# Kernel optimization log

Hardware: AMD Instinct MI355X
Metric: run time of the kernel (lower is better)

## Reference

```python
import jax, jax.numpy as jnp
import numpy as np

E = 1024   # embed_dim
H = 16     # num_heads
D = E // H # head_dim
T = 1024   # tgt_len
S = 1024   # src_len
B = 2      # batch
DELTA = 1.0
SCALE = D ** -0.5


def setup_inputs() -> dict:
    key = jax.random.key(0)
    ks = jax.random.split(key, 16)
    def lin(k, o, i):
        return jax.random.normal(k, (o, i), dtype=jnp.float32) / np.float32(np.sqrt(i))
    return {
        'query': jax.random.normal(ks[0], (T, B, E), dtype=jnp.float32),
        'key_in': jax.random.normal(ks[1], (S, B, E), dtype=jnp.float32),
        'value': jax.random.normal(ks[2], (S, B, E), dtype=jnp.float32),
        'Wq': lin(ks[3], E, E), 'bq': jnp.zeros((E,), jnp.float32),
        'Wk': lin(ks[4], E, E), 'bk': jnp.zeros((E,), jnp.float32),
        'Wv': lin(ks[5], E, E), 'bv': jnp.zeros((E,), jnp.float32),
        'Whq': lin(ks[6], E, E), 'bhq': jnp.zeros((E,), jnp.float32),
        'Whk': lin(ks[7], E, E), 'bhk': jnp.zeros((E,), jnp.float32),
        'Wwp': lin(ks[8], E, E), 'bwp': jnp.zeros((E,), jnp.float32),
        'Wvp': lin(ks[9], 1, E), 'bvp': jnp.zeros((1,), jnp.float32),
        'Wo': lin(ks[10], E, E), 'bo': jnp.zeros((E,), jnp.float32),
    }


def _heads(x, L):
    # (L, B, E) -> (B*H, L, D); E splits as (H, D) so flat index is b*H + h
    return x.reshape(L, B * H, D).transpose(1, 0, 2)


def reference(query, key_in, value, Wq, bq, Wk, bk, Wv, bv, Whq, bhq, Whk, bhk,
              Wwp, bwp, Wvp, bvp, Wo, bo):
    q = (query @ Wq.T + bq) * SCALE
    k = key_in @ Wk.T + bk
    v = value @ Wv.T + bv
    hq = query @ Whq.T + bhq
    hk = key_in @ Whk.T + bhk

    qh, hqh = _heads(q, T), _heads(hq, T)
    kh, hkh, vh = _heads(k, S), _heads(hk, S), _heads(v, S)

    # content attention logits  [B*H, T, S]
    attn = jnp.einsum('btd,bsd->bts', qh, kh)

    # Gaussian center: expected source position from hq/hk alignment
    align = jax.nn.softmax(jnp.einsum('btd,bsd->bts', hqh * SCALE, hkh), axis=-1)
    pos = jnp.arange(S, dtype=attn.dtype)          # index_mask
    mean = align @ pos                              # [B*H, T]

    # Gaussian width: per-query scalar via vp(tanh(wp(query)))
    g = (jnp.tanh(query @ Wwp.T + bwp) @ Wvp.T + bvp)[..., 0]   # (T, B)
    sigma = 1.0 + DELTA * jax.nn.sigmoid(g)                      # (T, B)
    sigma_bh = jnp.broadcast_to(sigma[:, :, None], (T, B, H)).reshape(T, B * H).T

    gauss = -((pos[None, None, :] - mean[:, :, None]) ** 2) / (
        2.0 * sigma_bh[:, :, None] ** 2)

    probs = jax.nn.softmax(attn + gauss, axis=-1)
    out = jnp.einsum('bts,bsd->btd', probs, vh)     # [B*H, T, D]
    out = out.transpose(1, 0, 2).reshape(T, B, E)
    return out @ Wo.T + bo
```

## Files before the change

### kernel.cpp

```cpp
#include <hip/hip_runtime.h>
#include <hip/hip_bf16.h>
#include <hip/hip_fp16.h>

#define T_ 1024
#define S_ 1024
#define B_ 2
#define H_ 16
#define D_ 64
#define E_ 1024
#define M_ (T_*B_)
#define SCALE_ 0.125f
#define LOG2E_ 1.4426950408889634f

typedef __attribute__((ext_vector_type(8))) short short8;
typedef __attribute__((ext_vector_type(8))) _Float16 half8;
typedef __attribute__((ext_vector_type(4))) float f32x4;

#define EXP2 __builtin_amdgcn_exp2f

__device__ __forceinline__ ushort f2bf(float x) {
  unsigned u = __float_as_uint(x);
  unsigned r = (u + 0x7fffu + ((u >> 16) & 1u)) >> 16;
  return (ushort)r;
}
__device__ __forceinline__ float bf2f(ushort h) {
  return __uint_as_float(((unsigned)h) << 16);
}
__device__ __forceinline__ ushort f2h(float x) {
  __half h = __float2half(x);
  return *(ushort*)&h;
}
__device__ __forceinline__ void gld16(const void* g, void* l) {
  __builtin_amdgcn_global_load_lds(
      (const __attribute__((address_space(1))) void*)g,
      (__attribute__((address_space(3))) void*)l, 16, 0, 0);
}
__device__ __forceinline__ unsigned cvtpk_bf16(float a, float b) {
  unsigned u;
  asm("v_cvt_pk_bf16_f32 %0, %1, %2" : "=v"(u) : "v"(a), "v"(b));
  return u;
}

#define SWZ(r, col) ((r)*64 + ((col) ^ (((r)&7)<<3)))

struct CvtDesc { const float* src; ushort* bf; ushort* h16; int n4; };
struct CvtArgs { CvtDesc d[10]; float* zero; int zn; };

__global__ __launch_bounds__(256) void cvt_kernel(CvtArgs a) {
  if (a.zero && blockIdx.y == 0) {
    for (int i = blockIdx.x*256 + threadIdx.x; i < a.zn; i += gridDim.x*256)
      a.zero[i] = 0.f;
  }
  const CvtDesc d = a.d[blockIdx.y];
  const int stride = gridDim.x * 256;
  for (int i = blockIdx.x*256 + threadIdx.x; i < d.n4; i += stride) {
    float4 v = ((const float4*)d.src)[i];
    float vals[4] = {v.x, v.y, v.z, v.w};
    if (d.bf) {
      ushort h[4];
      #pragma unroll
      for (int j = 0; j < 4; ++j) h[j] = f2bf(vals[j]);
      ((ushort4*)d.bf)[i] = make_ushort4(h[0],h[1],h[2],h[3]);
    }
    if (d.h16) {
      ushort h[4];
      #pragma unroll
      for (int j = 0; j < 4; ++j) h[j] = f2h(vals[j]);
      ((ushort4*)d.h16)[i] = make_ushort4(h[0],h[1],h[2],h[3]);
    }
  }
}

struct SegP { const ushort* A; const ushort* W; const float* bias;
              ushort* outb; float* outf; const float* vp; float scale; int flags; };
struct GemmArgs { SegP s[6]; };

template<int MT>
__global__ __launch_bounds__(256) void gemm_mfma(GemmArgs args) {
  constexpr int AG = MT/32;
  constexpr int MI = MT/32;
  constexpr int NY = 2048/MT;
  __shared__ ushort sA[MT*64];
  __shared__ ushort sW[64*64];
  const int id = blockIdx.x;
  const int xcd = id & 7, loc = id >> 3;
  const int x = xcd * ((gridDim.x >> 3) / NY) + loc / NY;
  const int y = loc % NY;
  const SegP sg = args.s[x >> 4];
  const int n0 = (x & 15) * 64;
  const int m0 = y * MT;
  const int tid = threadIdx.x, wv = tid >> 6, lane = tid & 63;
  const int c = lane & 15, g = lane >> 4;
  const int wr = wv >> 1, wc = wv & 1;
  const int lrow = lane >> 3;
  const int scol = ((lane & 7) ^ lrow) * 8;

  size_t aoff[AG], woff[2];
  #pragma unroll
  for (int j = 0; j < AG; ++j) {
    int rg = wv + j*4;
    aoff[j] = (size_t)(m0 + rg*8 + lrow)*1024 + scol;
  }
  #pragma unroll
  for (int j = 0; j < 2; ++j) {
    int rg = wv + j*4;
    woff[j] = (size_t)(n0 + rg*8 + lrow)*1024 + scol;
  }

  const bool isfp16 = (sg.flags & 2) != 0;
  f32x4 acc[MI][2] = {};
  for (int t = 0; t < 16; ++t) {
    const int k0 = t*64;
    #pragma unroll
    for (int j = 0; j < AG; ++j) {
      int rg = wv + j*4;
      gld16(sg.A + aoff[j] + k0, &sA[rg*512]);
    }
    #pragma unroll
    for (int j = 0; j < 2; ++j) {
      int rg = wv + j*4;
      gld16(sg.W + woff[j] + k0, &sW[rg*512]);
    }
    __syncthreads();
    #pragma unroll
    for (int ks = 0; ks < 2; ++ks) {
      short8 af[MI], wf[2];
      #pragma unroll
      for (int mi = 0; mi < MI; ++mi)
        af[mi] = *(const short8*)&sA[SWZ(wr*(MT/2) + mi*16 + c, ks*32 + g*8)];
      #pragma unroll
      for (int ni = 0; ni < 2; ++ni)
        wf[ni] = *(const short8*)&sW[SWZ(wc*32 + ni*16 + c, ks*32 + g*8)];
      if (isfp16) {
        #pragma unroll
        for (int mi = 0; mi < MI; ++mi)
          #pragma unroll
          for (int ni = 0; ni < 2; ++ni)
            acc[mi][ni] = __builtin_amdgcn_mfma_f32_16x16x32_f16(
                *(half8*)&af[mi], *(half8*)&wf[ni], acc[mi][ni], 0, 0, 0);
      } else {
        #pragma unroll
        for (int mi = 0; mi < MI; ++mi)
          #pragma unroll
          for (int ni = 0; ni < 2; ++ni)
            acc[mi][ni] = __builtin_amdgcn_mfma_f32_16x16x32_bf16(
                af[mi], wf[ni], acc[mi][ni], 0, 0, 0);
      }
    }
    __syncthreads();
  }

  if (sg.flags & 1) {
    const int col0 = n0 + wc*32 + c, col1 = col0 + 16;
    const float b0 = sg.bias[col0], b1 = sg.bias[col1];
    const float w0 = sg.vp[col0],  w1 = sg.vp[col1];
    #pragma unroll
    for (int mi = 0; mi < MI; ++mi) {
      #pragma unroll
      for (int r = 0; r < 4; ++r) {
        float v0 = tanhf((acc[mi][0][r] + b0) * sg.scale);
        float v1 = tanhf((acc[mi][1][r] + b1) * sg.scale);
        float part = v0*w0 + v1*w1;
        part += __shfl_xor(part, 1);
        part += __shfl_xor(part, 2);
        part += __shfl_xor(part, 4);
        part += __shfl_xor(part, 8);
        if (c == 0) {
          int row = m0 + wr*(MT/2) + mi*16 + 4*g + r;
          atomicAdd(&sg.outf[row], part);
        }
      }
    }
  } else {
    #pragma unroll
    for (int ni = 0; ni < 2; ++ni) {
      int col = n0 + wc*32 + ni*16 + c;
      float bias = sg.bias[col];
      #pragma unroll
      for (int mi = 0; mi < MI; ++mi) {
        #pragma unroll
        for (int r = 0; r < 4; ++r) {
          int row = m0 + wr*(MT/2) + mi*16 + 4*g + r;
          float val = (acc[mi][ni][r] + bias) * sg.scale;
          if (isfp16)       sg.outb[(size_t)row*1024 + col] = f2h(val);
          else if (sg.outf) sg.outf[(size_t)row*1024 + col] = val;
          else              sg.outb[(size_t)row*1024 + col] = f2bf(val);
        }
      }
    }
  }
}

__global__ __launch_bounds__(256) void attn_mfma(
    const ushort* __restrict__ q_bf, const ushort* __restrict__ k_bf,
    const ushort* __restrict__ v_bf,
    const ushort* __restrict__ hq_h16, const ushort* __restrict__ hk_h16,
    const float* __restrict__ sig_raw, const float* __restrict__ bvp,
    ushort* __restrict__ ctx) {
  __shared__ ushort sK[2][64*64];
  __shared__ ushort sV[2][64*64];
  __shared__ ushort sP[4*16*64];

  const int id = blockIdx.x;
  const int loc = id >> 3;
  const int bh = (id & 7) * 4 + (loc >> 4);
  const int b = bh >> 4, h = bh & 15;
  const int t0 = (loc & 15) * 64;
  const int tid = threadIdx.x;
  const int wv = tid >> 6, lane = tid & 63;
  const int c = lane & 15, g = lane >> 4;
  const int qbase = t0 + wv * 16;
  const size_t rowstr = (size_t)B_ * E_;
  const size_t qoff = ((size_t)(qbase + c) * B_ + b) * E_ + h * 64;

  short8 qf[2];
  half8  hqf[2];
  #pragma unroll
  for (int cs = 0; cs < 2; ++cs) {
    qf[cs]  = *(const short8*)&q_bf[qoff + cs*32 + g*8];
    hqf[cs] = *(const half8*)&hq_h16[qoff + cs*32 + g*8];
  }

  const int str0 = wv*16 + (lane >> 3);
  const int str1 = str0 + 8;
  const int chk0 = ((lane & 7) ^ (str0 & 7)) * 8;
  const int chk1 = ((lane & 7) ^ (str1 & 7)) * 8;
  const int ldsst = (wv*16) * 64;

  float den = 0.f, num = 0.f;
  {
    gld16(hk_h16 + ((size_t)str0 * B_ + b) * E_ + h*64 + chk0, &sK[0][ldsst]);
    gld16(hk_h16 + ((size_t)str1 * B_ + b) * E_ + h*64 + chk1, &sK[0][ldsst + 512]);
    __syncthreads();
    for (int t = 0; t < 16; ++t) {
      const ushort* kb = sK[t & 1];
      if (t < 15) {
        int s0n = (t+1) * 64;
        gld16(hk_h16 + ((size_t)(s0n + str0) * B_ + b) * E_ + h*64 + chk0,
              &sK[(t+1) & 1][ldsst]);
        gld16(hk_h16 + ((size_t)(s0n + str1) * B_ + b) * E_ + h*64 + chk1,
              &sK[(t+1) & 1][ldsst + 512]);
      }
      f32x4 acc[4] = {};
      __builtin_amdgcn_s_setprio(1);
      #pragma unroll
      for (int m = 0; m < 4; ++m)
        #pragma unroll
        for (int cs = 0; cs < 2; ++cs)
          acc[m] = __builtin_amdgcn_mfma_f32_16x16x32_f16(
              *(const half8*)&kb[SWZ(c + 16*m, cs*32 + g*8)], hqf[cs], acc[m], 0,0,0);
      __builtin_amdgcn_s_setprio(0);

      float fs = (float)(t*64 + 4*g);
      #pragma unroll
      for (int m = 0; m < 4; ++m)
        #pragma unroll
        for (int r = 0; r < 4; ++r) {
          float e = EXP2(acc[m][r]);
          den += e;
          num += e * (fs + (float)(16*m + r));
        }
      __syncthreads();
    }
  }
  den += __shfl_xor(den, 16); den += __shfl_xor(den, 32);
  num += __shfl_xor(num, 16); num += __shfl_xor(num, 32);
  const float meanq = num / den;
  const float graw = sig_raw[(size_t)(qbase + c) * B_ + b] + bvp[0];
  const float sgm = 1.f + 1.f/(1.f + __expf(-graw));
  const float fct = -LOG2E_ / (2.f * sgm * sgm);

  f32x4 accO[4] = {};
  float denq = 0.f;
  {
    gld16(k_bf + ((size_t)str0 * B_ + b) * E_ + h*64 + chk0, &sK[0][ldsst]);
    gld16(k_bf + ((size_t)str1 * B_ + b) * E_ + h*64 + chk1, &sK[0][ldsst + 512]);
    {
      int s2 = (tid & 31) * 2, d0 = (tid >> 5) * 8;
      size_t off0 = ((size_t)s2 * B_ + b) * E_ + h * 64 + d0;
      uint4 ra = *(const uint4*)&v_bf[off0];
      uint4 rb = *(const uint4*)&v_bf[off0 + rowstr];
      const ushort* pa = (const ushort*)&ra;
      const ushort* pb = (const ushort*)&rb;
      #pragma unroll
      for (int j = 0; j < 8; ++j)
        *(unsigned*)&sV[0][SWZ(d0 + j, s2)] = (unsigned)pa[j] | ((unsigned)pb[j] << 16);
    }
    __syncthreads();

    const int s2v = (tid & 31) * 2, d0v = (tid >> 5) * 8;
    for (int t = 0; t < 16; ++t) {
      const int cur = t & 1;
      const ushort* kb = sK[cur];
      const ushort* vb = sV[cur];
      uint4 ra, rb;
      if (t < 15) {
        int s0n = (t+1) * 64;
        gld16(k_bf + ((size_t)(s0n + str0) * B_ + b) * E_ + h*64 + chk0,
              &sK[cur^1][ldsst]);
        gld16(k_bf + ((size_t)(s0n + str1) * B_ + b) * E_ + h*64 + chk1,
              &sK[cur^1][ldsst + 512]);
        size_t off0 = ((size_t)(s0n + s2v) * B_ + b) * E_ + h * 64 + d0v;
        ra = *(const uint4*)&v_bf[off0];
        rb = *(const uint4*)&v_bf[off0 + rowstr];
      }

      f32x4 accL[4] = {};
      __builtin_amdgcn_s_setprio(1);
      #pragma unroll
      for (int m = 0; m < 4; ++m)
        #pragma unroll
        for (int cs = 0; cs < 2; ++cs)
          accL[m] = __builtin_amdgcn_mfma_f32_16x16x32_bf16(
              *(const short8*)&kb[SWZ(c + 16*m, cs*32 + g*8)], qf[cs], accL[m], 0,0,0);
      __builtin_amdgcn_s_setprio(0);

      float fs = (float)(t*64 + 4*g);
      float psum = 0.f;
      #pragma unroll
      for (int m = 0; m < 4; ++m) {
        float pr[4];
        #pragma unroll
        for (int r = 0; r < 4; ++r) {
          float dd = fs + (float)(16*m + r) - meanq;
          pr[r] = EXP2(accL[m][r] + fct * dd * dd);
          psum += pr[r];
        }
        uint2 uu;
        uu.x = cvtpk_bf16(pr[0], pr[1]);
        uu.y = cvtpk_bf16(pr[2], pr[3]);
        *(uint2*)&sP[wv*1024 + SWZ(c, 16*m + 4*g)] = uu;
      }
      denq += psum;

      __builtin_amdgcn_s_setprio(1);
      #pragma unroll
      for (int n = 0; n < 4; ++n)
        #pragma unroll
        for (int cs = 0; cs < 2; ++cs)
          accO[n] = __builtin_amdgcn_mfma_f32_16x16x32_bf16(
              *(const short8*)&sP[wv*1024 + SWZ(c, cs*32 + 8*g)],
              *(const short8*)&vb[SWZ(c + 16*n, cs*32 + 8*g)],
              accO[n], 0,0,0);
      __builtin_amdgcn_s_setprio(0);

      if (t < 15) {
        const ushort *pa = (const ushort*)&ra, *pb = (const ushort*)&rb;
        #pragma unroll
        for (int j = 0; j < 8; ++j)
          *(unsigned*)&sV[cur^1][SWZ(d0v + j, s2v)] = (unsigned)pa[j] | ((unsigned)pb[j] << 16);
      }
      __syncthreads();
    }
  }

  denq += __shfl_xor(denq, 16);
  denq += __shfl_xor(denq, 32);
  float dinv[4];
  #pragma unroll
  for (int r = 0; r < 4; ++r) dinv[r] = 1.f / __shfl(denq, 4*g + r);

  #pragma unroll
  for (int r = 0; r < 4; ++r) {
    size_t row = ((size_t)(qbase + 4*g + r) * B_ + b) * E_ + h * 64;
    #pragma unroll
    for (int n = 0; n < 4; ++n)
      ctx[row + 16*n + c] = f2bf(accO[n][r] * dinv[r]);
  }
}

extern "C" void kernel_launch(void* const* d_in, const int* in_sizes, int n_in,
                              void* d_out, int out_size, void* d_ws, size_t ws_size,
                              hipStream_t stream) {
  const float* query  = (const float*)d_in[0];
  const float* key_in = (const float*)d_in[1];
  const float* value  = (const float*)d_in[2];
  const float* Wq  = (const float*)d_in[3];  const float* bq  = (const float*)d_in[4];
  const float* Wk  = (const float*)d_in[5];  const float* bk  = (const float*)d_in[6];
  const float* Wv  = (const float*)d_in[7];  const float* bv  = (const float*)d_in[8];
  const float* Whq = (const float*)d_in[9];  const float* bhq = (const float*)d_in[10];
  const float* Whk = (const float*)d_in[11]; const float* bhk = (const float*)d_in[12];
  const float* Wwp = (const float*)d_in[13]; const float* bwp = (const float*)d_in[14];
  const float* Wvp = (const float*)d_in[15]; const float* bvp = (const float*)d_in[16];
  const float* Wo  = (const float*)d_in[17]; const float* bo  = (const float*)d_in[18];

  const size_t AU = (size_t)M_ * E_;
  const size_t WU = (size_t)E_ * E_;
  char* p = (char*)d_ws;
  float*  sig       = (float*)p;  p += 16384;
  ushort* query_bf  = (ushort*)p; p += AU*2;
  ushort* key_bf    = (ushort*)p; p += AU*2;
  ushort* value_bf  = (ushort*)p; p += AU*2;
  ushort* query_h16 = (ushort*)p; p += AU*2;
  ushort* key_h16   = (ushort*)p; p += AU*2;
  ushort* Whq_h16   = (ushort*)p; p += WU*2;
  ushort* Whk_h16   = (ushort*)p; p += WU*2;
  ushort* Wq_bf     = (ushort*)p; p += WU*2;
  ushort* Wk_bf     = (ushort*)p; p += WU*2;
  ushort* Wv_bf     = (ushort*)p; p += WU*2;
  ushort* Wwp_bf    = (ushort*)p; p += WU*2;
  ushort* Wo_bf     = (ushort*)p; p += WU*2;
  ushort* hq_h16    = (ushort*)p; p += AU*2;
  ushort* hk_h16    = (ushort*)p; p += AU*2;
  ushort* q_bf      = (ushort*)p; p += AU*2;
  ushort* k_bf      = (ushort*)p; p += AU*2;
  ushort* v_out     = (ushort*)p; p += AU*2;
  ushort* ctx_bf    = query_h16;

  {
    CvtArgs a{};
    a.d[0] = {query,  query_bf, query_h16, (int)(AU/4)};
    a.d[1] = {key_in, key_bf,   key_h16,   (int)(AU/4)};
    a.d[2] = {value,  value_bf, nullptr,   (int)(AU/4)};
    a.d[3] = {Whq,    nullptr,  Whq_h16,   (int)(WU/4)};
    a.d[4] = {Whk,    nullptr,  Whk_h16,   (int)(WU/4)};
    a.d[5] = {Wq,     Wq_bf,    nullptr,   (int)(WU/4)};
    a.d[6] = {Wk,     Wk_bf,    nullptr,   (int)(WU/4)};
    a.d[7] = {Wv,     Wv_bf,    nullptr,   (int)(WU/4)};
    a.d[8] = {Wwp,    Wwp_bf,   nullptr,   (int)(WU/4)};
    a.d[9] = {Wo,     Wo_bf,    nullptr,   (int)(WU/4)};
    a.zero = sig; a.zn = M_;
    cvt_kernel<<<dim3(128, 10), 256, 0, stream>>>(a);
  }
  {
    GemmArgs a{};
    a.s[0] = {query_bf,  Wq_bf,   bq,  q_bf,   nullptr, nullptr, SCALE_*LOG2E_, 0};
    a.s[1] = {query_bf,  Wwp_bf,  bwp, nullptr, sig,    Wvp,     1.f,           1};
    a.s[2] = {key_bf,    Wk_bf,   bk,  k_bf,   nullptr, nullptr, 1.f,           0};
    a.s[3] = {value_bf,  Wv_bf,   bv,  v_out,  nullptr, nullptr, 1.f,           0};
    a.s[4] = {query_h16, Whq_h16, bhq, hq_h16, nullptr, nullptr, SCALE_*LOG2E_, 2};
    a.s[5] = {key_h16,   Whk_h16, bhk, hk_h16, nullptr, nullptr, 1.f,           2};
    gemm_mfma<128><<<dim3(1536), 256, 0, stream>>>(a);
  }
  attn_mfma<<<dim3(512), 256, 0, stream>>>(
      q_bf, k_bf, v_out, hq_h16, hk_h16, sig, bvp, ctx_bf);
  {
    GemmArgs a{};
    a.s[0] = {ctx_bf, Wo_bf, bo, nullptr, (float*)d_out, nullptr, 1.f, 0};
    gemm_mfma<64><<<dim3(512), 256, 0, stream>>>(a);
  }
}
```

Before: 112.3 us.

## Double-buffer GEMM LDS tiles with async global loads two stages ahead

Converts the projection GEMM's single LDS buffer into a two-stage ping-pong buffer. Tiles are prefetched two K-steps ahead using direct-to-LDS loads, and explicit vmcnt waits replace the pair of __syncthreads per iteration. This lets global memory latency overlap with MFMA compute. It doubles LDS use, which may reduce occupancy, and correctness now depends on the hand-counted vmcnt values matching the number of outstanding loads per stage.

```diff
diff --git a/kernel.cpp b/kernel.cpp
--- a/kernel.cpp
+++ b/kernel.cpp
@@ -80,8 +80,8 @@
   constexpr int AG = MT/32;
   constexpr int MI = MT/32;
   constexpr int NY = 2048/MT;
-  __shared__ ushort sA[MT*64];
-  __shared__ ushort sW[64*64];
+  __shared__ ushort sA[2][MT*64];
+  __shared__ ushort sW[2][64*64];
   const int id = blockIdx.x;
   const int xcd = id & 7, loc = id >> 3;
   const int x = xcd * ((gridDim.x >> 3) / NY) + loc / NY;
@@ -107,30 +107,39 @@
     woff[j] = (size_t)(n0 + rg*8 + lrow)*1024 + scol;
   }
 
+  #define GSTAGE(buf, k0)                                       \
+    _Pragma("unroll")                                           \
+    for (int j = 0; j < AG; ++j)                                \
+      gld16(sg.A + aoff[j] + (k0), &sA[buf][(wv + j*4)*512]);   \
+    _Pragma("unroll")                                           \
+    for (int j = 0; j < 2; ++j)                                 \
+      gld16(sg.W + woff[j] + (k0), &sW[buf][(wv + j*4)*512]);
+
   const bool isfp16 = (sg.flags & 2) != 0;
   f32x4 acc[MI][2] = {};
+  GSTAGE(0, 0);
+  GSTAGE(1, 64);
+
   for (int t = 0; t < 16; ++t) {
-    const int k0 = t*64;
-    #pragma unroll
-    for (int j = 0; j < AG; ++j) {
-      int rg = wv + j*4;
-      gld16(sg.A + aoff[j] + k0, &sA[rg*512]);
-    }
-    #pragma unroll
-    for (int j = 0; j < 2; ++j) {
-      int rg = wv + j*4;
-      gld16(sg.W + woff[j] + k0, &sW[rg*512]);
-    }
-    __syncthreads();
+    const int cur = t & 1;
+    if (t < 15) {
+      if constexpr (MT == 128) asm volatile("s_waitcnt vmcnt(6)" ::: "memory");
+      else                     asm volatile("s_waitcnt vmcnt(4)" ::: "memory");
+    } else {
+      asm volatile("s_waitcnt vmcnt(0)" ::: "memory");
+    }
+    __builtin_amdgcn_s_barrier();
+    __builtin_amdgcn_sched_barrier(0);
+
     #pragma unroll
     for (int ks = 0; ks < 2; ++ks) {
       short8 af[MI], wf[2];
       #pragma unroll
       for (int mi = 0; mi < MI; ++mi)
-        af[mi] = *(const short8*)&sA[SWZ(wr*(MT/2) + mi*16 + c, ks*32 + g*8)];
+        af[mi] = *(const short8*)&sA[cur][SWZ(wr*(MT/2) + mi*16 + c, ks*32 + g*8)];
       #pragma unroll
       for (int ni = 0; ni < 2; ++ni)
-        wf[ni] = *(const short8*)&sW[SWZ(wc*32 + ni*16 + c, ks*32 + g*8)];
+        wf[ni] = *(const short8*)&sW[cur][SWZ(wc*32 + ni*16 + c, ks*32 + g*8)];
       if (isfp16) {
         #pragma unroll
         for (int mi = 0; mi < MI; ++mi)
@@ -147,8 +156,14 @@
                 af[mi], wf[ni], acc[mi][ni], 0, 0, 0);
       }
     }
-    __syncthreads();
-  }
+
+    if (t < 14) {
+      __builtin_amdgcn_sched_barrier(0);
+      __builtin_amdgcn_s_barrier();
+      GSTAGE(cur, (t+2)*64);
+    }
+  }
+  #undef GSTAGE
 
   if (sg.flags & 1) {
     const int col0 = n0 + wc*32 + c, col1 = col0 + 16;
```

After: 115.1 us. +2.5%, slower.
